# Kernel optimization log

Measured on AMD Instinct MI355X. Metric: run time of the kernel, lower is better.

Reference implementation:

```python
import jax, jax.numpy as jnp
import numpy as np

EPS = 1e-3  # Keras BatchNormalization default epsilon


def _conv2d_same(x, w):
    # x: [N,H,W,Cin], w: [kh,kw,Cin,Cout]
    return jax.lax.conv_general_dilated(
        x, w, window_strides=(1, 1), padding='SAME',
        dimension_numbers=('NHWC', 'HWIO', 'NHWC'))


def _hard_sigmoid(x):
    return jnp.clip(0.2 * x + 0.5, 0.0, 1.0)


def _convlstm2d(x, Wx, Wh, b):
    # x: [B,T,H,W,Cin]; Wx: [3,3,Cin,4F]; Wh: [3,3,F,4F]; b: [4F]
    B, T, H, W, Cin = x.shape
    F = Wh.shape[2]
    # precompute input-to-gate convs for all timesteps at once
    xg = _conv2d_same(x.reshape(B * T, H, W, Cin), Wx).reshape(B, T, H, W, 4 * F) + b

    def step(carry, xt):
        h, c = carry
        g = xt + _conv2d_same(h, Wh)
        gi, gf, gc, go = jnp.split(g, 4, axis=-1)  # Keras gate order i,f,c,o
        i = _hard_sigmoid(gi)
        f = _hard_sigmoid(gf)
        o = _hard_sigmoid(go)
        c = f * c + i * jnp.tanh(gc)
        h = o * jnp.tanh(c)
        return (h, c), h

    h0 = jnp.zeros((B, H, W, F), x.dtype)
    (_, _), hs = jax.lax.scan(step, (h0, h0), jnp.moveaxis(xg, 1, 0))
    return jnp.moveaxis(hs, 0, 1)  # [B,T,H,W,F]


def _batchnorm(x, g, be, m, v):
    # inference-mode BN over channel axis
    return (x - m) * (g * jax.lax.rsqrt(v + EPS)) + be


def setup_inputs() -> dict:
    key = jax.random.key(0)
    ks = jax.random.split(key, 10)
    B, T, H, W, C, F, NC = 16, 64, 16, 16, 6, 96, 10
    s = 0.05
    x = jax.random.normal(ks[0], (B, T, H, W, C), jnp.float32)
    Wx0 = jax.random.normal(ks[1], (3, 3, C, 4 * F), jnp.float32) * s
    Wh0 = jax.random.normal(ks[2], (3, 3, F, 4 * F), jnp.float32) * s
    b0 = jnp.zeros((4 * F,), jnp.float32)
    g0 = jnp.ones((F,), jnp.float32)
    be0 = jnp.zeros((F,), jnp.float32)
    m0 = jax.random.normal(ks[3], (F,), jnp.float32) * 0.1
    v0 = jax.random.uniform(ks[4], (F,), jnp.float32) + 0.5
    Wx1 = jax.random.normal(ks[5], (3, 3, F, 4 * F), jnp.float32) * s
    Wh1 = jax.random.normal(ks[6], (3, 3, F, 4 * F), jnp.float32) * s
    b1 = jnp.zeros((4 * F,), jnp.float32)
    g1 = jnp.ones((F,), jnp.float32)
    be1 = jnp.zeros((F,), jnp.float32)
    m1 = jax.random.normal(ks[7], (F,), jnp.float32) * 0.1
    v1 = jax.random.uniform(ks[8], (F,), jnp.float32) + 0.5
    Wd = jax.random.normal(ks[9], (T * H * W * F, NC), jnp.float32) * 0.001
    bd = jnp.zeros((NC,), jnp.float32)
    return dict(x=x, Wx0=Wx0, Wh0=Wh0, b0=b0, g0=g0, be0=be0, m0=m0, v0=v0,
                Wx1=Wx1, Wh1=Wh1, b1=b1, g1=g1, be1=be1, m1=m1, v1=v1,
                Wd=Wd, bd=bd)


def reference(x, Wx0, Wh0, b0, g0, be0, m0, v0,
              Wx1, Wh1, b1, g1, be1, m1, v1, Wd, bd):
    h = _convlstm2d(x, Wx0, Wh0, b0)
    h = _batchnorm(h, g0, be0, m0, v0)
    h = _convlstm2d(h, Wx1, Wh1, b1)
    h = _batchnorm(h, g1, be1, m1, v1)
    B = h.shape[0]
    flat = h.reshape(B, -1)  # Keras Flatten (row-major, channels-last)
    return flat @ Wd + bd
```

## Files before the change

### kernel.cpp

```cpp
#include <hip/hip_runtime.h>
#include <math.h>


typedef __attribute__((ext_vector_type(8))) short     bf16x8;
typedef __attribute__((ext_vector_type(8))) unsigned short u16x8;
typedef __attribute__((ext_vector_type(4))) float     f32x4;
typedef unsigned short u16;

#define RS 393216

__device__ __forceinline__ float hsig(float x) {
    return fminf(fmaxf(0.2f * x + 0.5f, 0.0f), 1.0f);
}
__device__ __forceinline__ float bf2f(u16 u) {
    union { unsigned int i; float f; } v; v.i = ((unsigned int)u) << 16; return v.f;
}
__device__ __forceinline__ u16 f2bf(float f) {
    union { float f; unsigned int i; } v; v.f = f;
    unsigned int r = (v.i + 0x7FFFu + ((v.i >> 16) & 1u)) >> 16;
    return (u16)r;
}

__device__ __forceinline__ void gridbar(unsigned* ctrs, unsigned* epoch,
                                        unsigned k, int blk)
{
    __syncthreads();
    if (threadIdx.x == 0) {
        __builtin_amdgcn_fence(__ATOMIC_RELEASE, "agent");
        __hip_atomic_fetch_add(ctrs + (blk & 63) * 64, 1u,
                               __ATOMIC_RELAXED, __HIP_MEMORY_SCOPE_AGENT);
    }
    if (blk == 0 && threadIdx.x < 64) {
        const unsigned target = k * 256u;
        unsigned sum;
        do {
            unsigned v = __hip_atomic_load(ctrs + threadIdx.x * 64,
                                           __ATOMIC_RELAXED,
                                           __HIP_MEMORY_SCOPE_AGENT);
            sum = v;
#pragma unroll
            for (int m = 1; m < 64; m <<= 1)
                sum += __shfl_xor(sum, m, 64);
            if (sum < target) __builtin_amdgcn_s_sleep(2);
        } while (sum < target);
        if (threadIdx.x == 0)
            __hip_atomic_store(epoch, k, __ATOMIC_RELAXED,
                               __HIP_MEMORY_SCOPE_AGENT);
    }
    if (threadIdx.x == 0) {
        while (__hip_atomic_load(epoch, __ATOMIC_RELAXED,
                                 __HIP_MEMORY_SCOPE_AGENT) < k)
            __builtin_amdgcn_s_sleep(4);
        __builtin_amdgcn_fence(__ATOMIC_ACQUIRE, "agent");
    }
    __syncthreads();
}

__device__ __forceinline__ void xbar(unsigned* slots, int myslot,
                                     unsigned target)
{
    __syncthreads();
    if (threadIdx.x == 0)
        __hip_atomic_fetch_add(slots + myslot * 32, 1u,
                               __ATOMIC_RELAXED, __HIP_MEMORY_SCOPE_AGENT);
    if (threadIdx.x < 32) {
        unsigned sum;
        do {
            unsigned v = __hip_atomic_load(slots + threadIdx.x * 32,
                                           __ATOMIC_RELAXED,
                                           __HIP_MEMORY_SCOPE_AGENT);
            sum = v;
#pragma unroll
            for (int m = 1; m < 32; m <<= 1)
                sum += __shfl_xor(sum, m, 64);
            if (sum < target) __builtin_amdgcn_s_sleep(2);
        } while (sum < target);
        asm volatile("buffer_inv sc0\n\ts_waitcnt vmcnt(0)" ::: "memory");
    }
    __syncthreads();
}

__global__ __launch_bounds__(256) void prep_x(const float* __restrict__ x,
                                              u16* __restrict__ xpad)
{
    const int idx = blockIdx.x * 256 + threadIdx.x;
    const int t = idx >> 12, b = (idx >> 8) & 15, p = idx & 255;
    const float* src = x + (((size_t)b * 64 + t) * 256 + p) * 6;
    u16x8 v = {};
    v[0] = f2bf(src[0]); v[1] = f2bf(src[1]); v[2] = f2bf(src[2]);
    v[3] = f2bf(src[3]); v[4] = f2bf(src[4]); v[5] = f2bf(src[5]);
    *(u16x8*)(xpad + (size_t)idx * 8) = v;
}

__global__ __launch_bounds__(256) void wtrans0(const float* __restrict__ Wx0,
                                               const float* __restrict__ Wh0,
                                               u16* __restrict__ Wt0)
{
    const int idx = blockIdx.x * 256 + threadIdx.x;
    const int n = idx / 960, k = idx - n * 960;
    const int nt = n / 96, j = n - nt * 96;
    const int no = (j / 24) * 96 + nt * 24 + (j % 24);
    float v = 0.0f;
    if (k < 96) {
        const int q = k >> 3, c = k & 7;
        if (q < 9 && c < 6) v = Wx0[(q * 6 + c) * 384 + no];
    } else {
        v = Wh0[(k - 96) * 384 + no];
    }
    Wt0[idx] = f2bf(v);
}

__global__ __launch_bounds__(256) void wtrans1(const float* __restrict__ Wx1,
                                               const float* __restrict__ Wh1,
                                               u16* __restrict__ Wt1)
{
    const int idx = blockIdx.x * 256 + threadIdx.x;
    const int n = idx / 1728, k = idx - n * 1728;
    const int nt = n / 96, j = n - nt * 96;
    const int no = (j / 24) * 96 + nt * 24 + (j % 24);
    const float v = (k < 864) ? Wx1[k * 384 + no] : Wh1[(k - 864) * 384 + no];
    Wt1[idx] = f2bf(v);
}

__global__ __launch_bounds__(256) void wtransD(const float* __restrict__ Wd,
                                               u16* __restrict__ WdT)
{
    const int k = blockIdx.x * 256 + threadIdx.x;
    const float* src = Wd + (size_t)k * 10;
#pragma unroll
    for (int nc = 0; nc < 10; ++nc)
        WdT[(size_t)nc * 1572864 + k] = f2bf(src[nc]);
}

__device__ void phase(int t, int m0, int n0, int tidx, char* lds,
    const u16* __restrict__ xpad, u16* __restrict__ h0b,
    u16* __restrict__ h1b, u16* __restrict__ h0bnb, u16* __restrict__ hall,
    const u16* __restrict__ Wt0, const u16* __restrict__ Wt1,
    const float* __restrict__ b0, const float* __restrict__ b1,
    const float* __restrict__ g0, const float* __restrict__ be0,
    const float* __restrict__ mu0, const float* __restrict__ v0,
    const float* __restrict__ g1, const float* __restrict__ be1,
    const float* __restrict__ mu1, const float* __restrict__ v1,
    float (&cregs)[6])
{
    const int half = tidx >> 8;
    const int htid = tidx & 255;
    const bool active = half ? (t < 63) : (t >= 0);

    const u16* in0 = half ? (xpad + (size_t)(t + 1) * 32768)
                          : (h0bnb + (size_t)(t & 1) * RS);
    const u16* in1 = half ? (h0b + (size_t)(t & 1) * RS)
                          : (h1b + (size_t)((t - 1) & 1) * RS);
    u16* hraw_out = half ? (h0b + (size_t)((t + 1) & 1) * RS)
                         : (h1b + (size_t)(t & 1) * RS);
    u16* hbn_out  = half ? (h0bnb + (size_t)((t + 1) & 1) * RS)
                         : (hall + (size_t)(t < 0 ? 0 : t) * RS);

    const int lane = htid & 63;
    const int hw   = htid >> 6;
    const int wm = hw >> 1, wn = hw & 1;
    const int fr = lane & 15, fg = lane >> 4;
    const int arow = htid >> 2, seg = htid & 3;
    const int mg = m0 + arow;
    const int py = (mg >> 4) & 15, px = mg & 15, pb = mg >> 8;
    const int nt = n0 / 96;

    const int   KT   = half ? 960 : 1728;
    const int   NS0  = half ? 3   : 27;
    const int   MYST = half ? 30  : 54;
    const u16*  Wt   = half ? Wt0 : Wt1;

    u16*   AsH  = (u16*)(lds + half * 51200);
    float* accS = (float*)(lds + half * 51200);

    f32x4 acc[2][3];
#pragma unroll
    for (int i = 0; i < 2; ++i)
#pragma unroll
        for (int j = 0; j < 3; ++j) acc[i][j] = (f32x4){0.f, 0.f, 0.f, 0.f};

    auto stage = [&](int ks, u16x8& va, u16x8& vb0, u16x8& vb1) {
        u16x8 z = {};
        va = z;
        if (half && ks < 3) {
            const int q = ks * 4 + seg;
            const int qd = q / 3;
            const int yy = py + qd - 1;
            const int xx = px + (q - 3 * qd) - 1;
            if (q < 9 && (unsigned)yy < 16u && (unsigned)xx < 16u)
                va = *(const u16x8*)(in0 + (size_t)((pb << 8) + yy * 16 + xx) * 8);
        } else {
            const int s = (ks < NS0) ? ks : ks - NS0;
            const u16* src = (ks < NS0) ? in0 : in1;
            const int q = s / 3;
            const int c0v = (s - 3 * q) * 32 + seg * 8;
            const int qd = q / 3;
            const int yy = py + qd - 1;
            const int xx = px + (q - 3 * qd) - 1;
            if ((unsigned)yy < 16u && (unsigned)xx < 16u)
                va = *(const u16x8*)(src + (size_t)((pb << 8) + yy * 16 + xx) * 96 + c0v);
        }
        const int koff = ks * 32 + seg * 8;
        vb0 = *(const u16x8*)(Wt + (size_t)(n0 + arow) * KT + koff);
        vb1 = z;
        if (htid < 128)
            vb1 = *(const u16x8*)(Wt + (size_t)(n0 + 64 + arow) * KT + koff);
    };
    auto ldsw = [&](int buf, u16x8& va, u16x8& vb0, u16x8& vb1) {
        u16* A = AsH + buf * 6400;
        u16* B = A + 2560;
        *(u16x8*)(A + arow * 40 + seg * 8) = va;
        *(u16x8*)(B + arow * 40 + seg * 8) = vb0;
        if (htid < 128) *(u16x8*)(B + (64 + arow) * 40 + seg * 8) = vb1;
    };
    auto dofrag = [&](int buf) {
        const u16* A = AsH + buf * 6400;
        const u16* B = A + 2560;
        bf16x8 af[2], bq[3];
#pragma unroll
        for (int mf = 0; mf < 2; ++mf)
            af[mf] = *(const bf16x8*)(A + (wm * 32 + mf * 16 + fr) * 40 + fg * 8);
#pragma unroll
        for (int nf = 0; nf < 3; ++nf)
            bq[nf] = *(const bf16x8*)(B + (wn * 48 + nf * 16 + fr) * 40 + fg * 8);

        __builtin_amdgcn_s_setprio(1);
#pragma unroll
        for (int mf = 0; mf < 2; ++mf)
#pragma unroll
            for (int nf = 0; nf < 3; ++nf)
                acc[mf][nf] = __builtin_amdgcn_mfma_f32_16x16x32_bf16(
                    af[mf], bq[nf], acc[mf][nf], 0, 0, 0);
        __builtin_amdgcn_s_setprio(0);
    };

    u16x8 vaA, vb0A, vb1A, vaB, vb0B, vb1B;

    if (active) {
        stage(0, vaA, vb0A, vb1A);
        stage(1, vaB, vb0B, vb1B);
        ldsw(0, vaA, vb0A, vb1A);
        ldsw(1, vaB, vb0B, vb1B);
    }
    __syncthreads();

    for (int j = 0; j < 27; ++j) {
        const int ks = 2 * j;
        if (active && ks < MYST) {
            const bool more = (ks + 2 < MYST);
            if (more) {
                stage(ks + 2, vaA, vb0A, vb1A);
                stage(ks + 3, vaB, vb0B, vb1B);
            }
            dofrag(ks & 3);
            dofrag((ks + 1) & 3);
            if (more) {
                ldsw((ks + 2) & 3, vaA, vb0A, vb1A);
                ldsw((ks + 3) & 3, vaB, vb0B, vb1B);
            }
        }
        __syncthreads();
    }

    if (active) {
        const float* bias = half ? b0 : b1;
#pragma unroll
        for (int nf = 0; nf < 3; ++nf) {
            const int col = wn * 48 + nf * 16 + fr;
            const float bi = bias[(col / 24) * 96 + nt * 24 + (col % 24)];
#pragma unroll
            for (int mf = 0; mf < 2; ++mf) {
                const int row = wm * 32 + mf * 16 + fg * 4;
#pragma unroll
                for (int r = 0; r < 4; ++r)
                    accS[(row + r) * 100 + col] = acc[mf][nf][r] + bi;
            }
        }
    }
    __syncthreads();

    if (active) {
        const float* gam = half ? g0 : g1;
        const float* bet = half ? be0 : be1;
        const float* muv = half ? mu0 : mu1;
        const float* var = half ? v0  : v1;
#pragma unroll
        for (int q = 0; q < 6; ++q) {
            const int item = htid + 256 * q;
            const int r = item / 24, fl = item - r * 24;
            const float gi = accS[r * 100 + fl];
            const float gf = accS[r * 100 + 24 + fl];
            const float gc = accS[r * 100 + 48 + fl];
            const float go = accS[r * 100 + 72 + fl];
            const int f = nt * 24 + fl;
            const float i_ = hsig(gi);
            const float f_ = hsig(gf);
            const float o_ = hsig(go);
            const float c_ = f_ * cregs[q] + i_ * tanhf(gc);
            const float h_ = o_ * tanhf(c_);
            cregs[q] = c_;
            hraw_out[(size_t)(m0 + r) * 96 + f] = f2bf(h_);
            const float s = gam[f] * rsqrtf(var[f] + 1e-3f);
            hbn_out[(size_t)(m0 + r) * 96 + f] =
                f2bf((h_ - muv[f]) * s + bet[f]);
        }
    }
}

__global__ __launch_bounds__(512, 2) void fused(
    unsigned* bctrs, unsigned* bepoch, unsigned* reg8, unsigned* xslots,
    const u16* xpad, u16* h0b, u16* h1b, u16* h0bnb, u16* hall,
    const u16* Wt0, const u16* Wt1,
    const float* b0, const float* b1,
    const float* g0, const float* be0, const float* mu0, const float* v0,
    const float* g1, const float* be1, const float* mu1, const float* v1)
{
    __shared__ char lds[102400];
    __shared__ unsigned shinfo[3];
    const int blk = blockIdx.x;

    if (threadIdx.x == 0) {
        unsigned xcc;
        asm volatile("s_getreg_b32 %0, hwreg(HW_REG_XCC_ID)" : "=s"(xcc));
        xcc &= 7u;
        unsigned slot = __hip_atomic_fetch_add(reg8 + xcc * 64, 1u,
                                               __ATOMIC_RELAXED,
                                               __HIP_MEMORY_SCOPE_AGENT);
        shinfo[0] = xcc; shinfo[1] = slot;
    }
    gridbar(bctrs, bepoch, 1, blk);
    if (threadIdx.x == 0) {
        unsigned ok = 1;
#pragma unroll
        for (int k = 0; k < 8; ++k)
            ok &= (__hip_atomic_load(reg8 + k * 64, __ATOMIC_RELAXED,
                                     __HIP_MEMORY_SCOPE_AGENT) == 32u);
        shinfo[2] = ok;
    }
    __syncthreads();
    const unsigned grp  = shinfo[0];
    const unsigned slot = shinfo[1];
    const bool grouped  = (shinfo[2] != 0u);

    float cregs[6] = {0.f, 0.f, 0.f, 0.f, 0.f, 0.f};

    if (grouped) {
        const int m0 = (int)grp * 512 + (int)(slot >> 2) * 64;
        const int n0 = (int)(slot & 3) * 96;
        unsigned* gs = xslots + grp * 1024;
        unsigned bar = 0;
        for (int t = -1; t < 64; ++t) {
            phase(t, m0, n0, threadIdx.x, lds, xpad, h0b, h1b, h0bnb, hall,
                  Wt0, Wt1, b0, b1, g0, be0, mu0, v0, g1, be1, mu1, v1, cregs);
            xbar(gs, (int)slot, (++bar) * 32u);
        }
    } else {
        const int m0 = (blk >> 2) * 64;
        const int n0 = (blk & 3) * 96;
        unsigned bar = 1;
        for (int t = -1; t < 64; ++t) {
            phase(t, m0, n0, threadIdx.x, lds, xpad, h0b, h1b, h0bnb, hall,
                  Wt0, Wt1, b0, b1, g0, be0, mu0, v0, g1, be1, mu1, v1, cregs);
            gridbar(bctrs, bepoch, ++bar, blk);
        }
    }
}

__global__ __launch_bounds__(512, 2) void stepF(int t,
    const u16* xpad, u16* h0b, u16* h1b, u16* h0bnb, u16* hall,
    const u16* Wt0, const u16* Wt1,
    const float* b0, const float* b1,
    const float* g0, const float* be0, const float* mu0, const float* v0,
    const float* g1, const float* be1, const float* mu1, const float* v1,
    float* c0g, float* c1g)
{
    __shared__ char lds[102400];
    const int m0 = (blockIdx.x >> 2) * 64;
    const int n0 = (blockIdx.x & 3) * 96;
    const int half = threadIdx.x >> 8;
    const int htid = threadIdx.x & 255;
    const int nt = n0 / 96;
    float* cst = half ? c0g : c1g;

    float cregs[6];
#pragma unroll
    for (int q = 0; q < 6; ++q) {
        const int item = htid + 256 * q;
        const int r = item / 24, fl = item - r * 24;
        cregs[q] = cst[(size_t)(m0 + r) * 96 + nt * 24 + fl];
    }
    phase(t, m0, n0, threadIdx.x, lds, xpad, h0b, h1b, h0bnb, hall,
          Wt0, Wt1, b0, b1, g0, be0, mu0, v0, g1, be1, mu1, v1, cregs);
#pragma unroll
    for (int q = 0; q < 6; ++q) {
        const int item = htid + 256 * q;
        const int r = item / 24, fl = item - r * 24;
        cst[(size_t)(m0 + r) * 96 + nt * 24 + fl] = cregs[q];
    }
}

__global__ void dense_partial(const u16* __restrict__ hall,
                              const u16* __restrict__ WdT,
                              float* __restrict__ partial)
{
    const int k0 = blockIdx.x * 2048;
    const int tt = k0 / 24576;
    const int r0 = k0 - tt * 24576;
    const int th = threadIdx.x;
    const int b  = th / 10;
    const int nc = th - b * 10;
    const u16* hp = hall + (size_t)(tt * 16 + b) * 24576 + r0;
    const u16* wp = WdT + (size_t)nc * 1572864 + k0;
    float acc = 0.0f;
    for (int j = 0; j < 2048; j += 8) {
        const u16x8 hv = *(const u16x8*)(hp + j);
        const u16x8 wv = *(const u16x8*)(wp + j);
#pragma unroll
        for (int u = 0; u < 8; ++u)
            acc = fmaf(bf2f(hv[u]), bf2f(wv[u]), acc);
    }
    partial[blockIdx.x * 160 + th] = acc;
}

__global__ void dense_reduce(const float* __restrict__ partial,
                             const float* __restrict__ bd,
                             float* __restrict__ out)
{
    const int t = threadIdx.x;
    const int nc = t - (t / 10) * 10;
    float acc = bd[nc];
    for (int p = 0; p < 768; ++p) acc += partial[p * 160 + t];
    out[t] = acc;
}

extern "C" void kernel_launch(void* const* d_in, const int* in_sizes, int n_in,
                              void* d_out, int out_size, void* d_ws, size_t ws_size,
                              hipStream_t stream)
{
    const float* x    = (const float*)d_in[0];
    const float* Wx0  = (const float*)d_in[1];
    const float* Wh0  = (const float*)d_in[2];
    const float* b0p  = (const float*)d_in[3];
    const float* g0p  = (const float*)d_in[4];
    const float* be0p = (const float*)d_in[5];
    const float* mu0p = (const float*)d_in[6];
    const float* v0p  = (const float*)d_in[7];
    const float* Wx1  = (const float*)d_in[8];
    const float* Wh1  = (const float*)d_in[9];
    const float* b1p  = (const float*)d_in[10];
    const float* g1p  = (const float*)d_in[11];
    const float* be1p = (const float*)d_in[12];
    const float* mu1p = (const float*)d_in[13];
    const float* v1p  = (const float*)d_in[14];
    const float* Wd   = (const float*)d_in[15];
    const float* bd   = (const float*)d_in[16];
    float* out = (float*)d_out;

    char* base = (char*)d_ws;
    u16*   h0b    = (u16*)(base);
    u16*   h1b    = (u16*)(base + 1572864);
    u16*   h0bnb  = (u16*)(base + 3145728);
    float* c0g    = (float*)(base + 4718592);
    float* c1g    = (float*)(base + 6291456);
    u16*   xpad   = (u16*)(base + 7864320);
    u16*   Wt0    = (u16*)(base + 12058624);
    u16*   Wt1    = (u16*)(base + 12795904);
    u16*   hall   = (u16*)(base + 14123008);
    float* part   = (float*)(base + 64454656);
    u16*   WdT    = (u16*)(base + 64946176);
    unsigned* bctrs  = (unsigned*)(base + 96403456);
    unsigned* bepoch = (unsigned*)(base + 96419840);
    unsigned* reg8   = (unsigned*)(base + 96420096);
    unsigned* xslots = (unsigned*)(base + 96422144);

    hipMemsetAsync(base, 0, 7864320, stream);
    hipMemsetAsync(bctrs, 0, 51456, stream);

    prep_x <<<1024, 256, 0, stream>>>(x, xpad);
    wtrans0<<<1440, 256, 0, stream>>>(Wx0, Wh0, Wt0);
    wtrans1<<<2592, 256, 0, stream>>>(Wx1, Wh1, Wt1);
    wtransD<<<6144, 256, 0, stream>>>(Wd, WdT);

    void* args[] = {
        (void*)&bctrs, (void*)&bepoch, (void*)&reg8, (void*)&xslots,
        (void*)&xpad, (void*)&h0b, (void*)&h1b, (void*)&h0bnb, (void*)&hall,
        (void*)&Wt0, (void*)&Wt1, (void*)&b0p, (void*)&b1p,
        (void*)&g0p, (void*)&be0p, (void*)&mu0p, (void*)&v0p,
        (void*)&g1p, (void*)&be1p, (void*)&mu1p, (void*)&v1p
    };
    hipError_t ce = hipLaunchCooperativeKernel((void*)fused, dim3(256),
                                               dim3(512), args, 0, stream);
    if (ce != hipSuccess) {
        (void)hipGetLastError();
        for (int t = -1; t < 64; ++t) {
            stepF<<<256, 512, 0, stream>>>(t, xpad, h0b, h1b, h0bnb, hall,
                                           Wt0, Wt1, b0p, b1p,
                                           g0p, be0p, mu0p, v0p,
                                           g1p, be1p, mu1p, v1p, c0g, c1g);
        }
    }

    dense_partial<<<768, 160, 0, stream>>>(hall, WdT, part);
    dense_reduce <<<1, 160, 0, stream>>>(part, bd, out);
}
```

Measured before the change: 1.922 ms.

## Pre-swizzle weights into MFMA fragment order and load B directly to registers

The weight transpose kernels now write the LSTM weights already laid out in per-lane MFMA B-fragment order, so the recurrent step loads B fragments straight from global memory into registers with double-buffered prefetch instead of staging them through LDS. This halves the LDS footprint (only A tiles are staged) and removes the LDS writes and reads for B. In exchange each wave issues more global loads per k-step and holds more fragment registers, and the launch bound drops from 2 to 1 blocks per SM, which changes register allocation limits.

```diff
diff --git a/kernel.cpp b/kernel.cpp
--- a/kernel.cpp
+++ b/kernel.cpp
@@ -92,14 +92,22 @@
     *(u16x8*)(xpad + (size_t)idx * 8) = v;
 }
 
-__global__ __launch_bounds__(256) void wtrans0(const float* __restrict__ Wx0,
-                                               const float* __restrict__ Wh0,
-                                               u16* __restrict__ Wt0)
+__global__ __launch_bounds__(256) void wtransF0(const float* __restrict__ Wx0,
+                                                const float* __restrict__ Wh0,
+                                                u16* __restrict__ W)
 {
     const int idx = blockIdx.x * 256 + threadIdx.x;
-    const int n = idx / 960, k = idx - n * 960;
-    const int nt = n / 96, j = n - nt * 96;
-    const int no = (j / 24) * 96 + nt * 24 + (j % 24);
+    const int e = idx & 7;
+    const int lane = (idx >> 3) & 63;
+    int r = idx >> 9;
+    const int nf = r % 3; r /= 3;
+    const int wn = r & 1; r >>= 1;
+    const int ks = r % 30;
+    const int nt = r / 30;
+    const int fr = lane & 15, fg = lane >> 4;
+    const int jl = wn * 48 + nf * 16 + fr;
+    const int no = (jl / 24) * 96 + nt * 24 + (jl % 24);
+    const int k = ks * 32 + fg * 8 + e;
     float v = 0.0f;
     if (k < 96) {
         const int q = k >> 3, c = k & 7;
@@ -107,19 +115,27 @@
     } else {
         v = Wh0[(k - 96) * 384 + no];
     }
-    Wt0[idx] = f2bf(v);
-}
-
-__global__ __launch_bounds__(256) void wtrans1(const float* __restrict__ Wx1,
-                                               const float* __restrict__ Wh1,
-                                               u16* __restrict__ Wt1)
+    W[idx] = f2bf(v);
+}
+
+__global__ __launch_bounds__(256) void wtransF1(const float* __restrict__ Wx1,
+                                                const float* __restrict__ Wh1,
+                                                u16* __restrict__ W)
 {
     const int idx = blockIdx.x * 256 + threadIdx.x;
-    const int n = idx / 1728, k = idx - n * 1728;
-    const int nt = n / 96, j = n - nt * 96;
-    const int no = (j / 24) * 96 + nt * 24 + (j % 24);
+    const int e = idx & 7;
+    const int lane = (idx >> 3) & 63;
+    int r = idx >> 9;
+    const int nf = r % 3; r /= 3;
+    const int wn = r & 1; r >>= 1;
+    const int ks = r % 54;
+    const int nt = r / 54;
+    const int fr = lane & 15, fg = lane >> 4;
+    const int jl = wn * 48 + nf * 16 + fr;
+    const int no = (jl / 24) * 96 + nt * 24 + (jl % 24);
+    const int k = ks * 32 + fg * 8 + e;
     const float v = (k < 864) ? Wx1[k * 384 + no] : Wh1[(k - 864) * 384 + no];
-    Wt1[idx] = f2bf(v);
+    W[idx] = f2bf(v);
 }
 
 __global__ __launch_bounds__(256) void wtransD(const float* __restrict__ Wd,
@@ -135,7 +151,7 @@
 __device__ void phase(int t, int m0, int n0, int tidx, char* lds,
     const u16* __restrict__ xpad, u16* __restrict__ h0b,
     u16* __restrict__ h1b, u16* __restrict__ h0bnb, u16* __restrict__ hall,
-    const u16* __restrict__ Wt0, const u16* __restrict__ Wt1,
+    const u16* __restrict__ WtF0, const u16* __restrict__ WtF1,
     const float* __restrict__ b0, const float* __restrict__ b1,
     const float* __restrict__ g0, const float* __restrict__ be0,
     const float* __restrict__ mu0, const float* __restrict__ v0,
@@ -165,13 +181,13 @@
     const int py = (mg >> 4) & 15, px = mg & 15, pb = mg >> 8;
     const int nt = n0 / 96;
 
-    const int   KT   = half ? 960 : 1728;
     const int   NS0  = half ? 3   : 27;
     const int   MYST = half ? 30  : 54;
-    const u16*  Wt   = half ? Wt0 : Wt1;
-
-    u16*   AsH  = (u16*)(lds + half * 51200);
-    float* accS = (float*)(lds + half * 51200);
+    const u16*  Bp   = (half ? WtF0 : WtF1)
+                       + (size_t)nt * (MYST * 3072) + wn * 1536 + (lane << 3);
+
+    u16*   AsH  = (u16*)(lds + half * 25600);
+    float* accS = (float*)(lds + half * 25600);
 
     f32x4 acc[2][3];
 #pragma unroll
@@ -179,7 +195,7 @@
 #pragma unroll
         for (int j = 0; j < 3; ++j) acc[i][j] = (f32x4){0.f, 0.f, 0.f, 0.f};
 
-    auto stage = [&](int ks, u16x8& va, u16x8& vb0, u16x8& vb1) {
+    auto stageA = [&](int ks, u16x8& va) {
         u16x8 z = {};
         va = z;
         if (half && ks < 3) {
@@ -200,29 +216,21 @@
             if ((unsigned)yy < 16u && (unsigned)xx < 16u)
                 va = *(const u16x8*)(src + (size_t)((pb << 8) + yy * 16 + xx) * 96 + c0v);
         }
-        const int koff = ks * 32 + seg * 8;
-        vb0 = *(const u16x8*)(Wt + (size_t)(n0 + arow) * KT + koff);
-        vb1 = z;
-        if (htid < 128)
-            vb1 = *(const u16x8*)(Wt + (size_t)(n0 + 64 + arow) * KT + koff);
     };
-    auto ldsw = [&](int buf, u16x8& va, u16x8& vb0, u16x8& vb1) {
-        u16* A = AsH + buf * 6400;
-        u16* B = A + 2560;
-        *(u16x8*)(A + arow * 40 + seg * 8) = va;
-        *(u16x8*)(B + arow * 40 + seg * 8) = vb0;
-        if (htid < 128) *(u16x8*)(B + (64 + arow) * 40 + seg * 8) = vb1;
+    auto ldswA = [&](int buf, u16x8& va) {
+        *(u16x8*)(AsH + buf * 2560 + arow * 40 + seg * 8) = va;
     };
-    auto dofrag = [&](int buf) {
-        const u16* A = AsH + buf * 6400;
-        const u16* B = A + 2560;
-        bf16x8 af[2], bq[3];
+    auto loadB = [&](int ks, bf16x8 (&bq)[3]) {
+#pragma unroll
+        for (int nf = 0; nf < 3; ++nf)
+            bq[nf] = *(const bf16x8*)(Bp + ks * 3072 + nf * 512);
+    };
+    auto dofrag = [&](int buf, bf16x8 (&bq)[3]) {
+        const u16* A = AsH + buf * 2560;
+        bf16x8 af[2];
 #pragma unroll
         for (int mf = 0; mf < 2; ++mf)
             af[mf] = *(const bf16x8*)(A + (wm * 32 + mf * 16 + fr) * 40 + fg * 8);
-#pragma unroll
-        for (int nf = 0; nf < 3; ++nf)
-            bq[nf] = *(const bf16x8*)(B + (wn * 48 + nf * 16 + fr) * 40 + fg * 8);
 
         __builtin_amdgcn_s_setprio(1);
 #pragma unroll
@@ -234,13 +242,13 @@
         __builtin_amdgcn_s_setprio(0);
     };
 
-    u16x8 vaA, vb0A, vb1A, vaB, vb0B, vb1B;
+    u16x8 vaA, vaB;
+    bf16x8 bqE[3], bqO[3], tE[3], tO[3];
 
     if (active) {
-        stage(0, vaA, vb0A, vb1A);
-        stage(1, vaB, vb0B, vb1B);
-        ldsw(0, vaA, vb0A, vb1A);
-        ldsw(1, vaB, vb0B, vb1B);
+        stageA(0, vaA); stageA(1, vaB);
+        ldswA(0, vaA);  ldswA(1, vaB);
+        loadB(0, bqE);  loadB(1, bqO);
     }
     __syncthreads();
 
@@ -249,14 +257,21 @@
         if (active && ks < MYST) {
             const bool more = (ks + 2 < MYST);
             if (more) {
-                stage(ks + 2, vaA, vb0A, vb1A);
-                stage(ks + 3, vaB, vb0B, vb1B);
+                stageA(ks + 2, vaA);
+                stageA(ks + 3, vaB);
+                loadB(ks + 2, tE);
+                loadB(ks + 3, tO);
             }
-            dofrag(ks & 3);
-            dofrag((ks + 1) & 3);
+            dofrag(ks & 3, bqE);
+            dofrag((ks + 1) & 3, bqO);
             if (more) {
-                ldsw((ks + 2) & 3, vaA, vb0A, vb1A);
-                ldsw((ks + 3) & 3, vaB, vb0B, vb1B);
+                ldswA((ks + 2) & 3, vaA);
+                ldswA((ks + 3) & 3, vaB);
+#pragma unroll
+                for (int nf = 0; nf < 3; ++nf) {
+                    bqE[nf] = tE[nf];
+                    bqO[nf] = tO[nf];
+                }
             }
         }
         __syncthreads();
@@ -307,15 +322,15 @@
     }
 }
 
-__global__ __launch_bounds__(512, 2) void fused(
+__global__ __launch_bounds__(512, 1) void fused(
     unsigned* bctrs, unsigned* bepoch, unsigned* reg8, unsigned* xslots,
     const u16* xpad, u16* h0b, u16* h1b, u16* h0bnb, u16* hall,
-    const u16* Wt0, const u16* Wt1,
+    const u16* WtF0, const u16* WtF1,
     const float* b0, const float* b1,
     const float* g0, const float* be0, const float* mu0, const float* v0,
     const float* g1, const float* be1, const float* mu1, const float* v1)
 {
-    __shared__ char lds[102400];
+    __shared__ char lds[51200];
     __shared__ unsigned shinfo[3];
     const int blk = blockIdx.x;
 
@@ -351,7 +366,8 @@
         unsigned bar = 0;
         for (int t = -1; t < 64; ++t) {
             phase(t, m0, n0, threadIdx.x, lds, xpad, h0b, h1b, h0bnb, hall,
-                  Wt0, Wt1, b0, b1, g0, be0, mu0, v0, g1, be1, mu1, v1, cregs);
+                  WtF0, WtF1, b0, b1, g0, be0, mu0, v0, g1, be1, mu1, v1,
+                  cregs);
             xbar(gs, (int)slot, (++bar) * 32u);
         }
     } else {
@@ -360,21 +376,22 @@
         unsigned bar = 1;
         for (int t = -1; t < 64; ++t) {
             phase(t, m0, n0, threadIdx.x, lds, xpad, h0b, h1b, h0bnb, hall,
-                  Wt0, Wt1, b0, b1, g0, be0, mu0, v0, g1, be1, mu1, v1, cregs);
+                  WtF0, WtF1, b0, b1, g0, be0, mu0, v0, g1, be1, mu1, v1,
+                  cregs);
             gridbar(bctrs, bepoch, ++bar, blk);
         }
     }
 }
 
-__global__ __launch_bounds__(512, 2) void stepF(int t,
+__global__ __launch_bounds__(512, 1) void stepF(int t,
     const u16* xpad, u16* h0b, u16* h1b, u16* h0bnb, u16* hall,
-    const u16* Wt0, const u16* Wt1,
+    const u16* WtF0, const u16* WtF1,
     const float* b0, const float* b1,
     const float* g0, const float* be0, const float* mu0, const float* v0,
     const float* g1, const float* be1, const float* mu1, const float* v1,
     float* c0g, float* c1g)
 {
-    __shared__ char lds[102400];
+    __shared__ char lds[51200];
     const int m0 = (blockIdx.x >> 2) * 64;
     const int n0 = (blockIdx.x & 3) * 96;
     const int half = threadIdx.x >> 8;
@@ -390,7 +407,7 @@
         cregs[q] = cst[(size_t)(m0 + r) * 96 + nt * 24 + fl];
     }
     phase(t, m0, n0, threadIdx.x, lds, xpad, h0b, h1b, h0bnb, hall,
-          Wt0, Wt1, b0, b1, g0, be0, mu0, v0, g1, be1, mu1, v1, cregs);
+          WtF0, WtF1, b0, b1, g0, be0, mu0, v0, g1, be1, mu1, v1, cregs);
 #pragma unroll
     for (int q = 0; q < 6; ++q) {
         const int item = htid + 256 * q;
@@ -463,8 +480,8 @@
     float* c0g    = (float*)(base + 4718592);
     float* c1g    = (float*)(base + 6291456);
     u16*   xpad   = (u16*)(base + 7864320);
-    u16*   Wt0    = (u16*)(base + 12058624);
-    u16*   Wt1    = (u16*)(base + 12795904);
+    u16*   WtF0   = (u16*)(base + 12058624);
+    u16*   WtF1   = (u16*)(base + 12795904);
     u16*   hall   = (u16*)(base + 14123008);
     float* part   = (float*)(base + 64454656);
     u16*   WdT    = (u16*)(base + 64946176);
@@ -476,15 +493,15 @@
     hipMemsetAsync(base, 0, 7864320, stream);
     hipMemsetAsync(bctrs, 0, 51456, stream);
 
-    prep_x <<<1024, 256, 0, stream>>>(x, xpad);
-    wtrans0<<<1440, 256, 0, stream>>>(Wx0, Wh0, Wt0);
-    wtrans1<<<2592, 256, 0, stream>>>(Wx1, Wh1, Wt1);
-    wtransD<<<6144, 256, 0, stream>>>(Wd, WdT);
+    prep_x  <<<1024, 256, 0, stream>>>(x, xpad);
+    wtransF0<<<1440, 256, 0, stream>>>(Wx0, Wh0, WtF0);
+    wtransF1<<<2592, 256, 0, stream>>>(Wx1, Wh1, WtF1);
+    wtransD <<<6144, 256, 0, stream>>>(Wd, WdT);
 
     void* args[] = {
         (void*)&bctrs, (void*)&bepoch, (void*)&reg8, (void*)&xslots,
         (void*)&xpad, (void*)&h0b, (void*)&h1b, (void*)&h0bnb, (void*)&hall,
-        (void*)&Wt0, (void*)&Wt1, (void*)&b0p, (void*)&b1p,
+        (void*)&WtF0, (void*)&WtF1, (void*)&b0p, (void*)&b1p,
         (void*)&g0p, (void*)&be0p, (void*)&mu0p, (void*)&v0p,
         (void*)&g1p, (void*)&be1p, (void*)&mu1p, (void*)&v1p
     };
@@ -494,7 +511,7 @@
         (void)hipGetLastError();
         for (int t = -1; t < 64; ++t) {
             stepF<<<256, 512, 0, stream>>>(t, xpad, h0b, h1b, h0bnb, hall,
-                                           Wt0, Wt1, b0p, b1p,
+                                           WtF0, WtF1, b0p, b1p,
                                            g0p, be0p, mu0p, v0p,
                                            g1p, be1p, mu1p, v1p, c0g, c1g);
         }
```

After: 1.743 ms. 1.1x faster.
